# Kernel tuning notes

Hardware: AMD Instinct MI355X
Metric: run time of the kernel (lower is better)

## Reference

```python
import jax, jax.numpy as jnp
import numpy as np

B, T, D_MODEL, N_HEADS = 2, 2048, 1024, 16


def setup_inputs() -> dict:
    key = jax.random.key(0)
    ks = jax.random.split(key, 5)
    w_scale = 0.02
    return {
        "x": jax.random.normal(ks[0], (B, T, D_MODEL), jnp.float32),
        "Wq": jax.random.normal(ks[1], (D_MODEL, D_MODEL), jnp.float32) * w_scale,
        "Wk": jax.random.normal(ks[2], (D_MODEL, D_MODEL), jnp.float32) * w_scale,
        "Wv": jax.random.normal(ks[3], (D_MODEL, D_MODEL), jnp.float32) * w_scale,
        "Wo": jax.random.normal(ks[4], (D_MODEL, D_MODEL), jnp.float32) * w_scale,
    }


def reference(x, Wq, Wk, Wv, Wo):
    Bv, Tv, _ = x.shape
    H = N_HEADS
    D = D_MODEL // H
    # Projections (torch nn.Linear: y = x @ W.T), split heads -> (B, H, T, D)
    q = (x @ Wq.T).reshape(Bv, Tv, H, D).transpose(0, 2, 1, 3)
    k = (x @ Wk.T).reshape(Bv, Tv, H, D).transpose(0, 2, 1, 3)
    v = (x @ Wv.T).reshape(Bv, Tv, H, D).transpose(0, 2, 1, 3)

    scale = jnp.sqrt(jnp.asarray(D, jnp.float32))
    scores = jnp.einsum("bhqd,bhkd->bhqk", q, k) / scale  # (B, H, T, T)

    # ALiBi bias: -|i-j| * slope_h, future positions masked to -inf (causal)
    slopes = jnp.asarray(
        [2.0 ** (-8.0 * h / H) for h in range(1, H + 1)], jnp.float32
    )
    pos = jnp.arange(Tv)
    dist = jnp.abs(pos[None, :] - pos[:, None]).astype(jnp.float32)  # (T, T)
    bias = -dist[None, :, :] * slopes[:, None, None]                 # (H, T, T)
    causal_mask = jnp.triu(jnp.ones((Tv, Tv), dtype=bool), 1)
    bias = jnp.where(causal_mask[None, :, :], -jnp.inf, bias)
    scores = scores + bias[None]  # (B, H, T, T)

    attn = jax.nn.softmax(scores, axis=-1)
    out = jnp.einsum("bhqk,bhkd->bhqd", attn, v)
    out = out.transpose(0, 2, 1, 3).reshape(Bv, Tv, D_MODEL)
    return out @ Wo.T
```

## Files before the change

### kernel.cpp

```cpp
#include <hip/hip_runtime.h>


#define DEV __device__ __forceinline__

typedef __attribute__((ext_vector_type(8))) short short8;
typedef __attribute__((ext_vector_type(4))) float f32x4;
typedef __attribute__((ext_vector_type(16))) float f32x16;
typedef __attribute__((ext_vector_type(4))) unsigned short ushort4v;
typedef __attribute__((ext_vector_type(4))) unsigned uint4v;

DEV unsigned short f2bf(float f) {
  unsigned u = __builtin_bit_cast(unsigned, f);
  u += 0x7fffu + ((u >> 16) & 1u);
  return (unsigned short)(u >> 16);
}
DEV float bf2f(unsigned short u) {
  unsigned x = ((unsigned)u) << 16;
  return __builtin_bit_cast(float, x);
}
DEV unsigned cvtpk_bf(float lo, float hi) {
  unsigned r;
  asm("v_cvt_pk_bf16_f32 %0, %1, %2" : "=v"(r) : "v"(lo), "v"(hi));
  return r;
}

DEV void gl2lds16(const void* g, void* l) {
  __builtin_amdgcn_global_load_lds(
      (const __attribute__((address_space(1))) void*)g,
      (__attribute__((address_space(3))) void*)l, 16, 0, 0);
}

__global__ __launch_bounds__(256) void cvt_all(
    const float* __restrict__ x, const float* __restrict__ wq,
    const float* __restrict__ wk, const float* __restrict__ wv,
    const float* __restrict__ wo, unsigned short* __restrict__ xb,
    unsigned short* __restrict__ wqb, unsigned short* __restrict__ wkb,
    unsigned short* __restrict__ wvb, unsigned short* __restrict__ wob) {
  int b = blockIdx.x;
  const float* s;
  unsigned short* d;
  int off;
  if (b < 4096)      { s = x;  d = xb;  off = b; }
  else if (b < 5120) { s = wq; d = wqb; off = b - 4096; }
  else if (b < 6144) { s = wk; d = wkb; off = b - 5120; }
  else if (b < 7168) { s = wv; d = wvb; off = b - 6144; }
  else               { s = wo; d = wob; off = b - 7168; }
  int i = (off * 256 + threadIdx.x) * 4;
  float4 v = *(const float4*)(s + i);
  ushort4v o = {f2bf(v.x), f2bf(v.y), f2bf(v.z), f2bf(v.w)};
  *(ushort4v*)(d + i) = o;
}

__global__ __launch_bounds__(512, 2) void gemm_qkv(
    const unsigned short* __restrict__ A, const unsigned short* __restrict__ Wq,
    const unsigned short* __restrict__ Wk, const unsigned short* __restrict__ Wv,
    unsigned short* __restrict__ Qo, unsigned short* __restrict__ Ko,
    unsigned short* __restrict__ Vo) {
  constexpr int K = 1024;
  __shared__ alignas(16) unsigned short Sm[65536];
  const int t = threadIdx.x;
  const int w = t >> 6, l = t & 63, l15 = l & 15, l4 = l >> 4;
  const int wr = w >> 2, wc = w & 3;
  const int wsel = blockIdx.x >> 2;
  const int n0 = (blockIdx.x & 3) * 256;
  const int m0 = blockIdx.y * 256;
  const unsigned short* Bmat = (wsel == 0) ? Wq : ((wsel == 1) ? Wk : Wv);

  const int srow = t >> 3;
  const int sk = ((t & 7) ^ (srow & 7)) * 8;

#define STG_A(T, H)                                                           \
  {                                                                           \
    gl2lds16(A + (m0 + (H)*128 + srow) * K + (T)*64 + sk,                     \
             &Sm[((T)&1) * 16384 + (H)*8192 + t * 8]);                        \
    gl2lds16(A + (m0 + (H)*128 + 64 + srow) * K + (T)*64 + sk,                \
             &Sm[((T)&1) * 16384 + (H)*8192 + 4096 + t * 8]);                 \
  }
#define STG_B(T, H)                                                           \
  {                                                                           \
    gl2lds16(Bmat + (n0 + (H)*128 + srow) * K + (T)*64 + sk,                  \
             &Sm[32768 + ((T)&1) * 16384 + (H)*8192 + t * 8]);                \
    gl2lds16(Bmat + (n0 + (H)*128 + 64 + srow) * K + (T)*64 + sk,             \
             &Sm[32768 + ((T)&1) * 16384 + (H)*8192 + 4096 + t * 8]);         \
  }

  f32x4 acc[8][4];
  {
    f32x4 z4 = {0.f, 0.f, 0.f, 0.f};
#pragma unroll
    for (int i = 0; i < 8; i++)
#pragma unroll
      for (int j = 0; j < 4; j++) acc[i][j] = z4;
  }
  short8 af[4][2], bf[2][2][2];

#define RD_AF(TT, QM)                                                         \
  {                                                                           \
    const unsigned short* Ab_ = &Sm[((TT)&1) * 16384];                        \
    _Pragma("unroll") for (int mi_ = 0; mi_ < 4; mi_++) {                     \
      _Pragma("unroll") for (int kk_ = 0; kk_ < 2; kk_++) {                   \
        af[mi_][kk_] = *(const short8*)&Ab_[                                  \
            (wr * 128 + (QM)*64 + mi_ * 16 + l15) * 64 +                      \
            (((kk_ * 4 + l4) ^ (l15 & 7)) * 8)];                              \
      }                                                                       \
    }                                                                         \
  }
#define RD_BF(TT, QN)                                                         \
  {                                                                           \
    const unsigned short* Bb_ = &Sm[32768 + ((TT)&1) * 16384];                \
    _Pragma("unroll") for (int ni_ = 0; ni_ < 2; ni_++) {                     \
      _Pragma("unroll") for (int kk_ = 0; kk_ < 2; kk_++) {                   \
        bf[(QN)][ni_][kk_] = *(const short8*)&Bb_[                            \
            (wc * 64 + (QN)*32 + ni_ * 16 + l15) * 64 +                       \
            (((kk_ * 4 + l4) ^ (l15 & 7)) * 8)];                              \
      }                                                                       \
    }                                                                         \
  }
#define DO_MFMA(QM, QN)                                                       \
  {                                                                           \
    _Pragma("unroll") for (int mi_ = 0; mi_ < 4; mi_++) {                     \
      _Pragma("unroll") for (int ni_ = 0; ni_ < 2; ni_++) {                   \
        _Pragma("unroll") for (int kk_ = 0; kk_ < 2; kk_++) {                 \
          acc[(QM)*4 + mi_][(QN)*2 + ni_] =                                   \
              __builtin_amdgcn_mfma_f32_16x16x32_bf16(                        \
                  af[mi_][kk_], bf[(QN)][ni_][kk_],                           \
                  acc[(QM)*4 + mi_][(QN)*2 + ni_], 0, 0, 0);                  \
        }                                                                     \
      }                                                                       \
    }                                                                         \
  }

#define VMW4 asm volatile("s_waitcnt vmcnt(4)" ::: "memory")
#define VMW0 asm volatile("s_waitcnt vmcnt(0)" ::: "memory")
#define NOW ((void)0)
#define PHASE(RDS, STG, MFMA_, WAIT)                                          \
  {                                                                           \
    RDS;                                                                      \
    STG;                                                                      \
    __builtin_amdgcn_s_barrier();                                             \
    __builtin_amdgcn_s_setprio(1);                                            \
    MFMA_;                                                                    \
    __builtin_amdgcn_s_setprio(0);                                            \
    WAIT;                                                                     \
    __builtin_amdgcn_s_barrier();                                             \
  }

  STG_B(0, 0); STG_B(0, 1); STG_A(0, 0); STG_A(0, 1);
  STG_B(1, 0); STG_B(1, 1);
  VMW4;
  __builtin_amdgcn_s_barrier();

#pragma unroll 1
  for (int i = 0; i < 7; ++i) {
    const int TA = 2 * i, TB = TA + 1;
    PHASE(RD_AF(TA, 0); RD_BF(TA, 0), STG_A(TB, 0),     DO_MFMA(0, 0), NOW);
    PHASE(RD_BF(TA, 1),               STG_A(TB, 1),     DO_MFMA(0, 1), NOW);
    PHASE(RD_AF(TA, 1),               STG_B(TA + 2, 0), DO_MFMA(1, 0), NOW);
    PHASE(NOW,                        STG_B(TA + 2, 1), DO_MFMA(1, 1), VMW4);
    PHASE(RD_AF(TB, 0); RD_BF(TB, 0), STG_A(TA + 2, 0), DO_MFMA(0, 0), NOW);
    PHASE(RD_BF(TB, 1),               STG_A(TA + 2, 1), DO_MFMA(0, 1), NOW);
    PHASE(RD_AF(TB, 1),               STG_B(TB + 2, 0), DO_MFMA(1, 0), NOW);
    PHASE(NOW,                        STG_B(TB + 2, 1), DO_MFMA(1, 1), VMW4);
  }
  PHASE(RD_AF(14, 0); RD_BF(14, 0), STG_A(15, 0), DO_MFMA(0, 0), NOW);
  PHASE(RD_BF(14, 1),               STG_A(15, 1), DO_MFMA(0, 1), NOW);
  PHASE(RD_AF(14, 1),               NOW,          DO_MFMA(1, 0), NOW);
  PHASE(NOW,                        NOW,          DO_MFMA(1, 1), VMW0);
  PHASE(RD_AF(15, 0); RD_BF(15, 0), NOW,          DO_MFMA(0, 0), NOW);
  PHASE(RD_BF(15, 1),               NOW,          DO_MFMA(0, 1), NOW);
  PHASE(RD_AF(15, 1),               NOW,          DO_MFMA(1, 0), NOW);
  PHASE(NOW,                        NOW,          DO_MFMA(1, 1), NOW);

#undef PHASE
#undef NOW
#undef VMW0
#undef VMW4
#undef DO_MFMA
#undef RD_BF
#undef RD_AF
#undef STG_B
#undef STG_A

  if (wsel != 2) {
    unsigned short* D = (wsel == 0) ? Qo : Ko;
    const float scale = (wsel == 0) ? 0.18033688011112042f : 1.0f;
    const int zb = (n0 >> 6) + wc;
#pragma unroll
    for (int mi = 0; mi < 8; mi++)
#pragma unroll
      for (int r = 0; r < 4; r++) {
        int m = m0 + wr * 128 + mi * 16 + l4 * 4 + r;
        int b = m >> 11, tt = m & 2047;
        int z = b * 16 + zb;
#pragma unroll
        for (int ni = 0; ni < 4; ni++)
          D[(z * 2048 + tt) * 64 + ni * 16 + l15] = f2bf(acc[mi][ni][r] * scale);
      }
  } else {
    unsigned short* Tr = Sm + w * 4608;
    const int b = (m0 + wr * 128) >> 11, tbase = (m0 + wr * 128) & 2047;
    const int zg = b * 16 + (n0 >> 6) + wc;
#pragma unroll
    for (int p = 0; p < 2; p++) {
#pragma unroll
      for (int mi = 0; mi < 4; mi++)
#pragma unroll
        for (int ni = 0; ni < 4; ni++) {
          int mg = p * 4 + mi;
          ushort4v pk = {f2bf(acc[mg][ni][0]), f2bf(acc[mg][ni][1]),
                         f2bf(acc[mg][ni][2]), f2bf(acc[mg][ni][3])};
          *(ushort4v*)&Tr[(ni * 16 + l15) * 72 + mi * 16 + l4 * 4] = pk;
        }
      asm volatile("s_waitcnt lgkmcnt(0)" ::: "memory");
      __builtin_amdgcn_sched_barrier(0);
#pragma unroll
      for (int j = 0; j < 8; j++) {
        int idx = j * 64 + l;
        int d = idx >> 3, c = idx & 7;
        int t0 = (c >> 1) * 16 + (c & 1) * 4;
        ushort4v lo4 = *(const ushort4v*)&Tr[d * 72 + t0];
        ushort4v hi4 = *(const ushort4v*)&Tr[d * 72 + t0 + 8];
        short8 v = {(short)lo4[0], (short)lo4[1], (short)lo4[2], (short)lo4[3],
                    (short)hi4[0], (short)hi4[1], (short)hi4[2], (short)hi4[3]};
        *(short8*)&Vo[(zg * 64 + d) * 2048 + tbase + p * 64 + c * 8] = v;
      }
      asm volatile("s_waitcnt lgkmcnt(0)" ::: "memory");
      __builtin_amdgcn_sched_barrier(0);
    }
  }
}

__global__ __launch_bounds__(256, 2) void gemm_o(
    const unsigned short* __restrict__ A, const unsigned short* __restrict__ Bm,
    float* __restrict__ C) {
  constexpr int K = 1024;
  __shared__ alignas(16) unsigned short Al[128 * 32];
  __shared__ alignas(16) unsigned short Bl[64 * 32];
  const int t = threadIdx.x;
  const int l = t & 63, l15 = l & 15, l4 = l >> 4;
  const int wm = ((t >> 6) & 1) * 64, wn = (t >> 7) * 32;
  const int sblk = (blockIdx.x & 7) * 64 + (blockIdx.x >> 3);
  const int m0 = (sblk >> 4) * 128, n0 = (sblk & 15) * 64;

  f32x4 zero4 = {0.f, 0.f, 0.f, 0.f};
  f32x4 acc[4][2];
#pragma unroll
  for (int i = 0; i < 4; i++)
#pragma unroll
    for (int j = 0; j < 2; j++) acc[i][j] = zero4;

  const int row0 = t >> 2, seg = (t & 3) * 8;
  const unsigned short* Ag0 = A + (m0 + row0) * K + seg;
  const unsigned short* Ag1 = A + (m0 + row0 + 64) * K + seg;
  const unsigned short* Bg0 = Bm + (n0 + row0) * K + seg;

  for (int k0 = 0; k0 < K; k0 += 32) {
    gl2lds16(Ag0 + k0, &Al[t * 8]);
    gl2lds16(Ag1 + k0, &Al[2048 + t * 8]);
    gl2lds16(Bg0 + k0, &Bl[t * 8]);
    __syncthreads();
    short8 af[4], bf2[2];
#pragma unroll
    for (int mi = 0; mi < 4; mi++)
      af[mi] = *(const short8*)&Al[(wm + mi * 16 + l15) * 32 + l4 * 8];
#pragma unroll
    for (int ni = 0; ni < 2; ni++)
      bf2[ni] = *(const short8*)&Bl[(wn + ni * 16 + l15) * 32 + l4 * 8];
#pragma unroll
    for (int mi = 0; mi < 4; mi++)
#pragma unroll
      for (int ni = 0; ni < 2; ni++)
        acc[mi][ni] = __builtin_amdgcn_mfma_f32_16x16x32_bf16(
            af[mi], bf2[ni], acc[mi][ni], 0, 0, 0);
    __syncthreads();
  }
#pragma unroll
  for (int mi = 0; mi < 4; mi++)
#pragma unroll
    for (int r = 0; r < 4; r++) {
      int m = m0 + wm + mi * 16 + l4 * 4 + r;
      float* cp = C + m * 1024 + n0 + wn + l15;
      cp[0] = acc[mi][0][r];
      cp[16] = acc[mi][1][r];
    }
}

__global__ __launch_bounds__(256, 3) void flash_alibi(
    const unsigned short* __restrict__ Q, const unsigned short* __restrict__ Kb,
    const unsigned short* __restrict__ Vt, unsigned short* __restrict__ Ob) {
  __shared__ alignas(16) unsigned short Kl[2 * 4096];
  __shared__ alignas(16) unsigned short Vl[2 * 4096];
  __shared__ float Lsh[128];
  const int t = threadIdx.x, w = t >> 6, l = t & 63;
  const int l31 = l & 31, h = l >> 5, lsw = l31 & 7;
  const int g = blockIdx.x;
  const int qt = 15 - (g >> 5);
  const int z = g & 31;
  const int q0 = qt * 128, hd = z & 15;
  const float slope2 = exp2f(-0.5f * (float)(hd + 1)) * 1.4426950408889634f;
  const int qrow = q0 + w * 32;
  const int qi = qrow + l31;

  short8 qf[4];
#pragma unroll
  for (int ks = 0; ks < 4; ks++)
    qf[ks] = *(const short8*)&Q[(z * 2048 + qi) * 64 + ks * 16 + h * 8];

  f32x16 binit;
#pragma unroll
  for (int r = 0; r < 16; r++)
    binit[r] =
        fmaf(slope2, (float)((r & 3) + 8 * (r >> 2) + 4 * h - qi), -10.0f);

  f32x16 accO[2];
  float lsum = 0.f;
#pragma unroll
  for (int nd = 0; nd < 2; nd++)
#pragma unroll
    for (int r = 0; r < 16; r++) accO[nd][r] = 0.f;

  const int sr = t >> 3, sgr = t & 7;
  const int nt = 2 * (qt + 1);

#define ISSUE_LOADS(KV0, BUF)                                                 \
  {                                                                           \
    unsigned short* Kd = &Kl[(BUF) * 4096];                                   \
    unsigned short* Vd = &Vl[(BUF) * 4096];                                   \
    const int sx = (sgr ^ (sr & 7)) * 8;                                      \
    gl2lds16(&Kb[(z * 2048 + (KV0) + sr) * 64 + sx], &Kd[t * 8]);             \
    gl2lds16(&Kb[(z * 2048 + (KV0) + 32 + sr) * 64 + sx],                     \
             &Kd[2048 + t * 8]);                                              \
    gl2lds16(&Vt[(z * 64 + sr) * 2048 + (KV0) + sx], &Vd[t * 8]);             \
    gl2lds16(&Vt[(z * 64 + 32 + sr) * 2048 + (KV0) + 32 + sx - 32],           \
             &Vd[2048 + t * 8]);                                              \
  }

  ISSUE_LOADS(0, 0)

  for (int ii = 0; ii < nt; ++ii) {
    __syncthreads();
    const int kv0 = ii * 64;
    if (ii + 1 < nt) ISSUE_LOADS(kv0 + 64, (ii + 1) & 1)
    if (kv0 > qrow + 31) continue;
    const unsigned short* Kc = &Kl[(ii & 1) * 4096];
    const unsigned short* Vc = &Vl[(ii & 1) * 4096];

    f32x16 accS[2];
    accS[0] = binit;
    accS[1] = binit;
#pragma unroll
    for (int ks = 0; ks < 4; ks++) {
      short8 kf0 =
          *(const short8*)&Kc[l31 * 64 + (((ks * 2 + h) ^ lsw) * 8)];
      short8 kf1 =
          *(const short8*)&Kc[(32 + l31) * 64 + (((ks * 2 + h) ^ lsw) * 8)];
      accS[0] = __builtin_amdgcn_mfma_f32_32x32x16_bf16(kf0, qf[ks], accS[0],
                                                        0, 0, 0);
      accS[1] = __builtin_amdgcn_mfma_f32_32x32x16_bf16(kf1, qf[ks], accS[1],
                                                        0, 0, 0);
    }

    const bool needMask = (kv0 + 63 > qrow);
#pragma unroll
    for (int ni = 0; ni < 2; ni++) {
      const float fkv = (float)(kv0 + 32 * ni);
      float ps[16];
#pragma unroll
      for (int r = 0; r < 16; r++)
        ps[r] = __builtin_amdgcn_exp2f(fmaf(slope2, fkv, accS[ni][r]));
      if (needMask) {
        const int kb = kv0 + 32 * ni + 4 * h;
#pragma unroll
        for (int r = 0; r < 16; r++)
          if (kb + ((r & 3) + 8 * (r >> 2)) > qi) ps[r] = 0.f;
      }
      lsum += (((ps[0] + ps[1]) + (ps[2] + ps[3])) +
               ((ps[4] + ps[5]) + (ps[6] + ps[7]))) +
              (((ps[8] + ps[9]) + (ps[10] + ps[11])) +
               ((ps[12] + ps[13]) + (ps[14] + ps[15])));
      unsigned pk[8];
#pragma unroll
      for (int i = 0; i < 8; i++) pk[i] = cvtpk_bf(ps[2 * i], ps[2 * i + 1]);
#pragma unroll
      for (int kp = 0; kp < 2; kp++) {
        uint4v pw = {pk[kp * 4 + 0], pk[kp * 4 + 1], pk[kp * 4 + 2],
                     pk[kp * 4 + 3]};
        short8 pa = __builtin_bit_cast(short8, pw);
#pragma unroll
        for (int nd = 0; nd < 2; nd++) {
          short8 vf = *(const short8*)&Vc[(nd * 32 + l31) * 64 +
                                          ((((ni * 2 + kp) * 2 + h) ^ lsw) * 8)];
          accO[nd] = __builtin_amdgcn_mfma_f32_32x32x16_bf16(pa, vf, accO[nd],
                                                             0, 0, 0);
        }
      }
    }
  }
#undef ISSUE_LOADS

  float lv = lsum + __shfl_xor(lsum, 32);
  float inv = 1.0f / lv;
  if (l < 32) Lsh[w * 32 + l31] = inv;
  asm volatile("s_waitcnt lgkmcnt(0)" ::: "memory");
  const int bq = z >> 4, hh = z & 15;
#pragma unroll
  for (int nd = 0; nd < 2; nd++)
#pragma unroll
    for (int r = 0; r < 16; r++) {
      int row = (r & 3) + 8 * (r >> 2) + 4 * h;
      int tg = qrow + row;
      float iv = Lsh[w * 32 + row];
      Ob[(bq * 2048 + tg) * 1024 + hh * 64 + nd * 32 + l31] =
          f2bf(accO[nd][r] * iv);
    }
}

extern "C" void kernel_launch(void* const* d_in, const int* in_sizes, int n_in,
                              void* d_out, int out_size, void* d_ws,
                              size_t ws_size, hipStream_t stream) {
  const float* x = (const float*)d_in[0];
  const float* Wq = (const float*)d_in[1];
  const float* Wk = (const float*)d_in[2];
  const float* Wv = (const float*)d_in[3];
  const float* Wo = (const float*)d_in[4];

  char* p = (char*)d_ws;
  unsigned short* xb = (unsigned short*)p;  p += 4096 * 1024 * 2;
  unsigned short* wqb = (unsigned short*)p; p += 1024 * 1024 * 2;
  unsigned short* wkb = (unsigned short*)p; p += 1024 * 1024 * 2;
  unsigned short* wvb = (unsigned short*)p; p += 1024 * 1024 * 2;
  unsigned short* wob = (unsigned short*)p; p += 1024 * 1024 * 2;
  unsigned short* Qb = (unsigned short*)p;  p += 32 * 2048 * 64 * 2;
  unsigned short* Kbf = (unsigned short*)p; p += 32 * 2048 * 64 * 2;
  unsigned short* Vtb = (unsigned short*)p; p += 32 * 2048 * 64 * 2;
  unsigned short* Ob = (unsigned short*)p;  p += 32 * 2048 * 64 * 2;

  cvt_all<<<8192, 256, 0, stream>>>(x, Wq, Wk, Wv, Wo, xb, wqb, wkb, wvb, wob);
  gemm_qkv<<<dim3(12, 16), 512, 0, stream>>>(xb, wqb, wkb, wvb, Qb, Kbf, Vtb);
  flash_alibi<<<512, 256, 0, stream>>>(Qb, Kbf, Vtb, Ob);
  gemm_o<<<512, 256, 0, stream>>>(Ob, wob, (float*)d_out);
}
```

Baseline: 174.6 us.

## Split attention KV range across two blocks with flag-synced partial merge

Each query tile's causal KV range is now split in half between two workgroups. The first finisher writes its unnormalized partial output and row sums to a workspace and raises a flag. The second spins on that flag, then merges and normalizes. Flags are zeroed in the conversion kernel. This doubles the grid to improve load balance and occupancy on the long causal tiles, and also raises the occupancy hint and adds s_setprio around the MFMA sections. The cost is extra partial-output traffic, a bf16 rounding of the partial result, and spin-wait dependence between co-resident blocks.

```diff
diff --git a/kernel.cpp b/kernel.cpp
--- a/kernel.cpp
+++ b/kernel.cpp
@@ -8,6 +8,7 @@
 typedef __attribute__((ext_vector_type(16))) float f32x16;
 typedef __attribute__((ext_vector_type(4))) unsigned short ushort4v;
 typedef __attribute__((ext_vector_type(4))) unsigned uint4v;
+typedef __attribute__((ext_vector_type(4))) int int4v;
 
 DEV unsigned short f2bf(float f) {
   unsigned u = __builtin_bit_cast(unsigned, f);
@@ -35,8 +36,13 @@
     const float* __restrict__ wk, const float* __restrict__ wv,
     const float* __restrict__ wo, unsigned short* __restrict__ xb,
     unsigned short* __restrict__ wqb, unsigned short* __restrict__ wkb,
-    unsigned short* __restrict__ wvb, unsigned short* __restrict__ wob) {
+    unsigned short* __restrict__ wvb, unsigned short* __restrict__ wob,
+    int* __restrict__ flags) {
   int b = blockIdx.x;
+  if (b == 8191) {
+    int4v z4 = {0, 0, 0, 0};
+    ((int4v*)flags)[threadIdx.x] = z4;
+  }
   const float* s;
   unsigned short* d;
   int off;
@@ -285,17 +291,20 @@
     }
 }
 
-__global__ __launch_bounds__(256, 3) void flash_alibi(
+__global__ __launch_bounds__(256, 4) void flash_alibi(
     const unsigned short* __restrict__ Q, const unsigned short* __restrict__ Kb,
-    const unsigned short* __restrict__ Vt, unsigned short* __restrict__ Ob) {
+    const unsigned short* __restrict__ Vt, unsigned short* __restrict__ Opart,
+    float* __restrict__ Lpart, int* __restrict__ flags,
+    unsigned short* __restrict__ Ob) {
   __shared__ alignas(16) unsigned short Kl[2 * 4096];
   __shared__ alignas(16) unsigned short Vl[2 * 4096];
   __shared__ float Lsh[128];
+  __shared__ int role_sh;
   const int t = threadIdx.x, w = t >> 6, l = t & 63;
   const int l31 = l & 31, h = l >> 5, lsw = l31 & 7;
   const int g = blockIdx.x;
-  const int qt = 15 - (g >> 5);
-  const int z = g & 31;
+  const int qt = 15 - (g >> 6);
+  const int z = (g & 63) >> 1, s = g & 1;
   const int q0 = qt * 128, hd = z & 15;
   const float slope2 = exp2f(-0.5f * (float)(hd + 1)) * 1.4426950408889634f;
   const int qrow = q0 + w * 32;
@@ -320,7 +329,8 @@
     for (int r = 0; r < 16; r++) accO[nd][r] = 0.f;
 
   const int sr = t >> 3, sgr = t & 7;
-  const int nt = 2 * (qt + 1);
+  const int it0 = s ? (qt + 1) : 0;
+  const int nt = qt + 1;
 
 #define ISSUE_LOADS(KV0, BUF)                                                 \
   {                                                                           \
@@ -331,15 +341,15 @@
     gl2lds16(&Kb[(z * 2048 + (KV0) + 32 + sr) * 64 + sx],                     \
              &Kd[2048 + t * 8]);                                              \
     gl2lds16(&Vt[(z * 64 + sr) * 2048 + (KV0) + sx], &Vd[t * 8]);             \
-    gl2lds16(&Vt[(z * 64 + 32 + sr) * 2048 + (KV0) + 32 + sx - 32],           \
+    gl2lds16(&Vt[(z * 64 + 32 + sr) * 2048 + (KV0) + sx],                     \
              &Vd[2048 + t * 8]);                                              \
   }
 
-  ISSUE_LOADS(0, 0)
+  ISSUE_LOADS(it0 * 64, 0)
 
   for (int ii = 0; ii < nt; ++ii) {
     __syncthreads();
-    const int kv0 = ii * 64;
+    const int kv0 = (it0 + ii) * 64;
     if (ii + 1 < nt) ISSUE_LOADS(kv0 + 64, (ii + 1) & 1)
     if (kv0 > qrow + 31) continue;
     const unsigned short* Kc = &Kl[(ii & 1) * 4096];
@@ -348,6 +358,7 @@
     f32x16 accS[2];
     accS[0] = binit;
     accS[1] = binit;
+    __builtin_amdgcn_s_setprio(1);
 #pragma unroll
     for (int ks = 0; ks < 4; ks++) {
       short8 kf0 =
@@ -359,6 +370,7 @@
       accS[1] = __builtin_amdgcn_mfma_f32_32x32x16_bf16(kf1, qf[ks], accS[1],
                                                         0, 0, 0);
     }
+    __builtin_amdgcn_s_setprio(0);
 
     const bool needMask = (kv0 + 63 > qrow);
 #pragma unroll
@@ -381,6 +393,7 @@
       unsigned pk[8];
 #pragma unroll
       for (int i = 0; i < 8; i++) pk[i] = cvtpk_bf(ps[2 * i], ps[2 * i + 1]);
+      __builtin_amdgcn_s_setprio(1);
 #pragma unroll
       for (int kp = 0; kp < 2; kp++) {
         uint4v pw = {pk[kp * 4 + 0], pk[kp * 4 + 1], pk[kp * 4 + 2],
@@ -394,25 +407,52 @@
                                                              0, 0, 0);
         }
       }
+      __builtin_amdgcn_s_setprio(0);
     }
   }
 #undef ISSUE_LOADS
 
+  const int p = g >> 1;
   float lv = lsum + __shfl_xor(lsum, 32);
-  float inv = 1.0f / lv;
-  if (l < 32) Lsh[w * 32 + l31] = inv;
-  asm volatile("s_waitcnt lgkmcnt(0)" ::: "memory");
-  const int bq = z >> 4, hh = z & 15;
-#pragma unroll
-  for (int nd = 0; nd < 2; nd++)
-#pragma unroll
-    for (int r = 0; r < 16; r++) {
-      int row = (r & 3) + 8 * (r >> 2) + 4 * h;
-      int tg = qrow + row;
-      float iv = Lsh[w * 32 + row];
-      Ob[(bq * 2048 + tg) * 1024 + hh * 64 + nd * 32 + l31] =
-          f2bf(accO[nd][r] * iv);
+  if (t == 0) role_sh = atomicAdd(&flags[p * 2], 1);
+  __syncthreads();
+  const int role = role_sh;
+  unsigned short* Po = Opart + p * 128 * 64;
+  float* Pl = Lpart + p * 128;
+
+  if (role == 0) {
+    if (l < 32) Pl[w * 32 + l31] = lv;
+#pragma unroll
+    for (int nd = 0; nd < 2; nd++)
+#pragma unroll
+      for (int r = 0; r < 16; r++) {
+        int row = (r & 3) + 8 * (r >> 2) + 4 * h;
+        Po[(w * 32 + row) * 64 + nd * 32 + l31] = f2bf(accO[nd][r]);
+      }
+    __threadfence();
+    __syncthreads();
+    if (t == 0) atomicExch(&flags[p * 2 + 1], 1);
+  } else {
+    if (t == 0) {
+      while (atomicAdd(&flags[p * 2 + 1], 0) == 0) __builtin_amdgcn_s_sleep(2);
     }
+    __syncthreads();
+    __threadfence();
+    if (l < 32) Lsh[w * 32 + l31] = lv + Pl[w * 32 + l31];
+    asm volatile("s_waitcnt lgkmcnt(0)" ::: "memory");
+    const int bq = z >> 4, hh = z & 15;
+#pragma unroll
+    for (int nd = 0; nd < 2; nd++)
+#pragma unroll
+      for (int r = 0; r < 16; r++) {
+        int row = (r & 3) + 8 * (r >> 2) + 4 * h;
+        int tg = qrow + row;
+        float ov = bf2f(Po[(w * 32 + row) * 64 + nd * 32 + l31]);
+        float iv = 1.0f / Lsh[w * 32 + row];
+        Ob[(bq * 2048 + tg) * 1024 + hh * 64 + nd * 32 + l31] =
+            f2bf((accO[nd][r] + ov) * iv);
+      }
+  }
 }
 
 extern "C" void kernel_launch(void* const* d_in, const int* in_sizes, int n_in,
@@ -433,10 +473,14 @@
   unsigned short* Qb = (unsigned short*)p;  p += 32 * 2048 * 64 * 2;
   unsigned short* Kbf = (unsigned short*)p; p += 32 * 2048 * 64 * 2;
   unsigned short* Vtb = (unsigned short*)p; p += 32 * 2048 * 64 * 2;
+  unsigned short* Opart = (unsigned short*)p; p += 512 * 128 * 64 * 2;
   unsigned short* Ob = (unsigned short*)p;  p += 32 * 2048 * 64 * 2;
-
-  cvt_all<<<8192, 256, 0, stream>>>(x, Wq, Wk, Wv, Wo, xb, wqb, wkb, wvb, wob);
+  float* Lpart = (float*)p;                 p += 512 * 128 * 4;
+  int* flags = (int*)p;                     p += 1024 * 4;
+
+  cvt_all<<<8192, 256, 0, stream>>>(x, Wq, Wk, Wv, Wo, xb, wqb, wkb, wvb, wob,
+                                    flags);
   gemm_qkv<<<dim3(12, 16), 512, 0, stream>>>(xb, wqb, wkb, wvb, Qb, Kbf, Vtb);
-  flash_alibi<<<512, 256, 0, stream>>>(Qb, Kbf, Vtb, Ob);
+  flash_alibi<<<1024, 256, 0, stream>>>(Qb, Kbf, Vtb, Opart, Lpart, flags, Ob);
   gemm_o<<<512, 256, 0, stream>>>(Ob, wob, (float*)d_out);
 }
```

Measured after the change: 284.5 us. +63.0%, slower.
